# Kernel optimization log

Measured on AMD Instinct MI355X. Metric: run time of the kernel, lower is better.

Reference implementation:

```python
import jax, jax.numpy as jnp
import numpy as np

N = 50000      # nodes
E = 1600000    # edges (before self-loops)
F_IN = 160     # input feature dim
H = 8          # heads
C = 8          # per-head channels
HC = H * C     # 64
G = 64         # graphs in batch
NEG_SLOPE = 0.2


def setup_inputs() -> dict:
    key = jax.random.key(0)
    ks = jax.random.split(key, 20)
    x = jax.random.normal(ks[0], (N, F_IN), jnp.float32)
    edge_index = jax.random.randint(ks[1], (2, E), 0, N, dtype=jnp.int64)
    batch = jnp.sort(jax.random.randint(ks[2], (N,), 0, G, dtype=jnp.int64))

    def w(k, shape):
        fan = shape[0] + shape[-1]
        lim = np.sqrt(6.0 / fan).astype(np.float32)
        return jax.random.uniform(k, shape, jnp.float32, -lim, lim)

    return {
        "x": x, "edge_index": edge_index, "batch": batch,
        "W1": w(ks[3], (F_IN, HC)), "a1s": w(ks[4], (H, C)), "a1d": w(ks[5], (H, C)), "b1": jnp.zeros((HC,), jnp.float32),
        "W2": w(ks[6], (HC, HC)),   "a2s": w(ks[7], (H, C)), "a2d": w(ks[8], (H, C)), "b2": jnp.zeros((HC,), jnp.float32),
        "W3": w(ks[9], (HC, HC)),   "a3s": w(ks[10], (H, C)), "a3d": w(ks[11], (H, C)), "b3": jnp.zeros((HC,), jnp.float32),
        "Wlin": w(ks[12], (HC, 2)), "blin": jnp.zeros((2,), jnp.float32),
    }


def gat_layer(x, src, dst, W, a_src, a_dst, b):
    # h: [N, H, C]
    h = (x @ W).reshape(-1, H, C)
    alpha_src = jnp.einsum('nhc,hc->nh', h, a_src)  # [N, H]
    alpha_dst = jnp.einsum('nhc,hc->nh', h, a_dst)  # [N, H]
    # per-edge scores: message from src j to dst i (PyG convention)
    e = jax.nn.leaky_relu(alpha_src[src] + alpha_dst[dst], NEG_SLOPE)  # [Et, H]
    # softmax over incoming edges of each dst node (numerically stable)
    m = jax.ops.segment_max(e, dst, num_segments=N)
    ex = jnp.exp(e - m[dst])
    s = jax.ops.segment_sum(ex, dst, num_segments=N)
    a = ex / (s[dst] + 1e-16)                                          # [Et, H]
    out = jax.ops.segment_sum(h[src] * a[:, :, None], dst, num_segments=N)
    return out.reshape(-1, HC) + b


def reference(x, edge_index, batch, W1, a1s, a1d, b1, W2, a2s, a2d, b2,
              W3, a3s, a3d, b3, Wlin, blin):
    # add self-loops (PyG GATConv default)
    loop = jnp.arange(N, dtype=edge_index.dtype)
    src = jnp.concatenate([edge_index[0], loop])
    dst = jnp.concatenate([edge_index[1], loop])

    h = jax.nn.elu(gat_layer(x, src, dst, W1, a1s, a1d, b1))
    h = jax.nn.elu(gat_layer(h, src, dst, W2, a2s, a2d, b2))
    h = jax.nn.elu(gat_layer(h, src, dst, W3, a3s, a3d, b3))

    # global mean pool over graphs
    sums = jax.ops.segment_sum(h, batch, num_segments=G)               # [G, HC]
    cnt = jax.ops.segment_sum(jnp.ones((h.shape[0], 1), h.dtype), batch, num_segments=G)
    pooled = sums / jnp.maximum(cnt, 1.0)

    logits = pooled @ Wlin + blin                                      # [G, 2]
    return jax.nn.log_softmax(logits, axis=1)
```

## Files before the change

### kernel.cpp

```cpp
#include <hip/hip_runtime.h>
#include <hip/hip_bf16.h>

#define NNODES 50000
#define NEDGES 1600000
#define F_IN   160
#define NHEAD  8
#define HC     64
#define NGRAPH 64
#define NEG_SLOPE 0.2f

#define BW2   256
#define NB2   ((NNODES + BW2 - 1) / BW2)
#define BCAP  12288
#define EPB   8192
#define PA_BLOCKS ((NEDGES + EPB - 1) / EPB)
#define EPT   (EPB / 256)
#define PCCAP 12288
#define SCAN_BLK 49

__global__ void __launch_bounds__(256) partA_kernel(const int* __restrict__ ei,
                                                    int* __restrict__ bcur,
                                                    unsigned* __restrict__ stage) {
    __shared__ int cnt[NB2];
    __shared__ int rb[NB2];
    __shared__ int gb[NB2];
    __shared__ int sc[256];
    __shared__ unsigned stg[EPB];
    int t = threadIdx.x;
    int e0 = blockIdx.x * EPB;
    for (int i = t; i < NB2; i += 256) cnt[i] = 0;
    __syncthreads();

    unsigned pck[EPT];
#pragma unroll
    for (int i = 0; i < EPT; i++) {
        int e = e0 + i * 256 + t;
        if (e < NEDGES) {
            int s = ei[e];
            int d = ei[NEDGES + e];
            int b = d >> 8;
            pck[i] = (unsigned)s | ((unsigned)(d & 255) << 16) | ((unsigned)b << 24);
            atomicAdd(&cnt[b], 1);
        } else {
            pck[i] = 0xFFFFFFFFu;
        }
    }
    __syncthreads();
    int c = (t < NB2) ? cnt[t] : 0;
    sc[t] = c;
    __syncthreads();
    for (int d = 1; d < 256; d <<= 1) {
        int v = (t >= d) ? sc[t - d] : 0;
        __syncthreads();
        sc[t] += v;
        __syncthreads();
    }
    if (t < NB2) {
        rb[t] = sc[t] - c;
        gb[t] = (c > 0) ? atomicAdd(&bcur[t], c) : 0;
        cnt[t] = 0;
    }
    __syncthreads();
#pragma unroll
    for (int i = 0; i < EPT; i++) {
        int b = pck[i] >> 24;
        if (b < NB2) {
            int p = rb[b] + atomicAdd(&cnt[b], 1);
            stg[p] = pck[i];
        }
    }
    __syncthreads();
    int total = sc[255];
    for (int idx = t; idx < total; idx += 256) {
        unsigned v = stg[idx];
        int b = v >> 24;
        int pos = gb[b] + (idx - rb[b]);
        if (pos < BCAP) stage[(size_t)b * BCAP + pos] = v;
    }
}

__global__ void __launch_bounds__(256) partB_kernel(const unsigned* __restrict__ stage,
                                                    const int* __restrict__ bcur,
                                                    int* __restrict__ deg, int N) {
    __shared__ int cnt[BW2];
    int b = blockIdx.x, t = threadIdx.x;
    cnt[t] = 0;
    __syncthreads();
    int n = bcur[b]; if (n > BCAP) n = BCAP;
    const unsigned* sg = stage + (size_t)b * BCAP;
    for (int i = t; i < n; i += 256) atomicAdd(&cnt[(sg[i] >> 16) & 255], 1);
    __syncthreads();
    int node = b * BW2 + t;
    if (node < N) deg[node] = cnt[t];
}

__global__ void scan_partial_kernel(const int* __restrict__ deg, int* __restrict__ psum, int N) {
    __shared__ int red[256];
    int tid = threadIdx.x;
    int i4 = blockIdx.x * 256 + tid;
    int n4 = N / 4;
    int s = 0;
    if (i4 < n4) {
        int4 v = ((const int4*)deg)[i4];
        s = v.x + v.y + v.z + v.w + 4;
    }
    red[tid] = s;
    __syncthreads();
    for (int d = 128; d > 0; d >>= 1) {
        if (tid < d) red[tid] += red[tid + d];
        __syncthreads();
    }
    if (tid == 0) psum[blockIdx.x] = red[0];
}

__global__ void scan_base_kernel(const int* __restrict__ psum, int* __restrict__ pbase) {
    int lane = threadIdx.x;
    int v = (lane < SCAN_BLK) ? psum[lane] : 0;
    int own = v;
    for (int off = 1; off < 64; off <<= 1) {
        int u = __shfl_up(v, off);
        if (lane >= off) v += u;
    }
    if (lane < SCAN_BLK) pbase[lane] = v - own;
}

__global__ void scan_write_kernel(const int* __restrict__ deg, const int* __restrict__ pbase,
                                  int* __restrict__ row_ptr, int N) {
    __shared__ int red[256];
    int tid = threadIdx.x;
    int b = blockIdx.x;
    int i4 = b * 256 + tid;
    int n4 = N / 4;
    int4 v = make_int4(0, 0, 0, 0);
    int s = 0;
    if (i4 < n4) {
        v = ((const int4*)deg)[i4];
        s = v.x + v.y + v.z + v.w + 4;
    }
    red[tid] = s;
    __syncthreads();
    for (int d = 1; d < 256; d <<= 1) {
        int t2 = (tid >= d) ? red[tid - d] : 0;
        __syncthreads();
        red[tid] += t2;
        __syncthreads();
    }
    if (i4 < n4) {
        int base = pbase[b] + red[tid] - s;
        int gi = i4 * 4;
        int r0 = base + v.x + 1;
        int r1 = r0 + v.y + 1;
        int r2 = r1 + v.z + 1;
        int r3 = r2 + v.w + 1;
        row_ptr[gi + 1] = r0;
        row_ptr[gi + 2] = r1;
        row_ptr[gi + 3] = r2;
        row_ptr[gi + 4] = r3;
        if (gi == 0) row_ptr[0] = 0;
    }
}

__global__ void __launch_bounds__(256) partC_kernel(const unsigned* __restrict__ stage,
                                                    const int* __restrict__ bcur,
                                                    const int* __restrict__ row_ptr,
                                                    int* __restrict__ csr, int N) {
    __shared__ int rstart[BW2 + 1];
    __shared__ int lfill[BW2];
    __shared__ int ord[PCCAP];
    int b = blockIdx.x, t = threadIdx.x;
    int n0 = b * BW2;
    lfill[t] = 0;
    { int n = n0 + t; rstart[t] = row_ptr[n < N ? n : N]; }
    if (t == 0) { int n = n0 + BW2; rstart[BW2] = row_ptr[n < N ? n : N]; }
    __syncthreads();
    int base0 = rstart[0];
    int total = rstart[BW2] - base0;
    int cnt = bcur[b]; if (cnt > BCAP) cnt = BCAP;
    const unsigned* sg = stage + (size_t)b * BCAP;
    if (total <= PCCAP) {
        for (int i = t; i < cnt; i += 256) {
            unsigned v = sg[i];
            int dl = (v >> 16) & 255;
            int p = (rstart[dl] - base0) + atomicAdd(&lfill[dl], 1);
            ord[p] = v & 0xFFFF;
        }
        __syncthreads();
        { int n = n0 + t; if (n < N) ord[rstart[t + 1] - 1 - base0] = n; }
        __syncthreads();
        for (int i = t; i < total; i += 256) csr[base0 + i] = ord[i];
    } else {
        for (int i = t; i < cnt; i += 256) {
            unsigned v = sg[i];
            int dl = (v >> 16) & 255;
            int p = rstart[dl] + atomicAdd(&lfill[dl], 1);
            csr[p] = v & 0xFFFF;
        }
        __syncthreads();
        { int n = n0 + t; if (n < N) csr[rstart[t + 1] - 1] = n; }
    }
}

template <int K, int KC>
__global__ void __launch_bounds__(256) gemm_tile_kernel(const float* __restrict__ in,
                                                        const float* __restrict__ W,
                                                        const float* __restrict__ aS,
                                                        const float* __restrict__ aD,
                                                        __hip_bfloat16* __restrict__ h_out,
                                                        float* __restrict__ alpha_s,
                                                        float* __restrict__ alpha_d,
                                                        int N) {
    __shared__ float xs[64][KC + 1];
    __shared__ float Wl[KC][64];
    int t = threadIdx.x;
    int n0 = blockIdx.x * 64;
    int tn = (t >> 4) << 2;
    int tc = (t & 15) << 2;
    float acc[4][4] = {};

    for (int kc = 0; kc < K; kc += KC) {
        for (int idx = t; idx < 64 * (KC / 4); idx += 256) {
            int n = idx / (KC / 4);
            int k4 = (idx - n * (KC / 4)) * 4;
            int node = n0 + n;
            float4 v = make_float4(0.f, 0.f, 0.f, 0.f);
            if (node < N) v = *reinterpret_cast<const float4*>(&in[(size_t)node * K + kc + k4]);
            xs[n][k4 + 0] = v.x;
            xs[n][k4 + 1] = v.y;
            xs[n][k4 + 2] = v.z;
            xs[n][k4 + 3] = v.w;
        }
        for (int idx = t; idx < KC * 16; idx += 256) {
            int k = idx >> 4;
            int c4 = (idx & 15) << 2;
            *reinterpret_cast<float4*>(&Wl[k][c4]) =
                *reinterpret_cast<const float4*>(&W[(size_t)(kc + k) * HC + c4]);
        }
        __syncthreads();
#pragma unroll 8
        for (int k = 0; k < KC; k++) {
            float x0 = xs[tn + 0][k];
            float x1 = xs[tn + 1][k];
            float x2 = xs[tn + 2][k];
            float x3 = xs[tn + 3][k];
            float4 wv = *reinterpret_cast<const float4*>(&Wl[k][tc]);
            acc[0][0] = fmaf(x0, wv.x, acc[0][0]);
            acc[0][1] = fmaf(x0, wv.y, acc[0][1]);
            acc[0][2] = fmaf(x0, wv.z, acc[0][2]);
            acc[0][3] = fmaf(x0, wv.w, acc[0][3]);
            acc[1][0] = fmaf(x1, wv.x, acc[1][0]);
            acc[1][1] = fmaf(x1, wv.y, acc[1][1]);
            acc[1][2] = fmaf(x1, wv.z, acc[1][2]);
            acc[1][3] = fmaf(x1, wv.w, acc[1][3]);
            acc[2][0] = fmaf(x2, wv.x, acc[2][0]);
            acc[2][1] = fmaf(x2, wv.y, acc[2][1]);
            acc[2][2] = fmaf(x2, wv.z, acc[2][2]);
            acc[2][3] = fmaf(x2, wv.w, acc[2][3]);
            acc[3][0] = fmaf(x3, wv.x, acc[3][0]);
            acc[3][1] = fmaf(x3, wv.y, acc[3][1]);
            acc[3][2] = fmaf(x3, wv.z, acc[3][2]);
            acc[3][3] = fmaf(x3, wv.w, acc[3][3]);
        }
        __syncthreads();
    }

#pragma unroll
    for (int i = 0; i < 4; i++) {
        int node = n0 + tn + i;
        if (node < N) {
            __hip_bfloat16 tmp[4];
            tmp[0] = __float2bfloat16(acc[i][0]);
            tmp[1] = __float2bfloat16(acc[i][1]);
            tmp[2] = __float2bfloat16(acc[i][2]);
            tmp[3] = __float2bfloat16(acc[i][3]);
            *reinterpret_cast<ushort4*>(&h_out[(size_t)node * HC + tc]) =
                *reinterpret_cast<const ushort4*>(tmp);
        }
    }

    float4 aSv = *reinterpret_cast<const float4*>(&aS[tc]);
    float4 aDv = *reinterpret_cast<const float4*>(&aD[tc]);
    float ps[4], pd[4];
#pragma unroll
    for (int i = 0; i < 4; i++) {
        ps[i] = acc[i][0] * aSv.x + acc[i][1] * aSv.y + acc[i][2] * aSv.z + acc[i][3] * aSv.w;
        pd[i] = acc[i][0] * aDv.x + acc[i][1] * aDv.y + acc[i][2] * aDv.z + acc[i][3] * aDv.w;
    }
#pragma unroll
    for (int i = 0; i < 4; i++) {
        ps[i] += __shfl_xor(ps[i], 1);
        pd[i] += __shfl_xor(pd[i], 1);
    }
    if ((t & 1) == 0) {
        int head = (t & 15) >> 1;
#pragma unroll
        for (int i = 0; i < 4; i++) {
            int node = n0 + tn + i;
            if (node < N) {
                alpha_s[node * NHEAD + head] = ps[i];
                alpha_d[node * NHEAD + head] = pd[i];
            }
        }
    }
}

__global__ void __launch_bounds__(256) agg_kernel(const __hip_bfloat16* __restrict__ h,
                           const float* __restrict__ as_, const float* __restrict__ ad_,
                           const int* __restrict__ rowp, const int* __restrict__ csr,
                           const float* __restrict__ bias, float* __restrict__ out, int N) {
    int tid = threadIdx.x;
    int node = blockIdx.x * 4 + (tid >> 6);
    if (node >= N) return;
    int lane = tid & 63;
    int head = lane >> 3;
    int j8 = lane & 7;
    int bl = lane & 56;

    int beg = rowp[node], end = rowp[node + 1];
    int deg = end - beg;
    float adn = ad_[node * NHEAD + head];

    float num0 = 0.f, num1 = 0.f, dent = 0.f;
    int s0safe = csr[beg];
    int ngrp = (deg + 7) >> 3;
    for (int g = 0; g < ngrp; g++) {
        int eidx = g * 8 + j8;
        int sE = s0safe;
        float w_t = 0.f;
        if (eidx < deg) {
            sE = csr[beg + eidx];
            float e = as_[sE * NHEAD + head] + adn;
            e = (e > 0.f) ? e : NEG_SLOPE * e;
            w_t = __expf(e);
        }
        dent += w_t;
#pragma unroll
        for (int j = 0; j < 8; j += 2) {
            int   sa = __shfl(sE, bl + j);
            float wa = __shfl(w_t, bl + j);
            float ha = __bfloat162float(h[(size_t)sa * HC + lane]);
            num0 = fmaf(wa, ha, num0);
            int   sb = __shfl(sE, bl + j + 1);
            float wb = __shfl(w_t, bl + j + 1);
            float hb = __bfloat162float(h[(size_t)sb * HC + lane]);
            num1 = fmaf(wb, hb, num1);
        }
    }
    dent += __shfl_xor(dent, 1);
    dent += __shfl_xor(dent, 2);
    dent += __shfl_xor(dent, 4);
    float o = (num0 + num1) / (dent + 1e-16f) + bias[lane];
    out[node * HC + lane] = (o > 0.f) ? o : (__expf(o) - 1.f);
}

#define PCH 64
__global__ void __launch_bounds__(256) pool_kernel(const float* __restrict__ h,
                                                   const int* __restrict__ batch,
                                                   float* __restrict__ pooled, int N) {
    int tid = threadIdx.x;
    int lane = tid & 63, w = tid >> 6;
    int base = blockIdx.x * PCH + w * (PCH / 4);
    if (base >= N) return;
    int end = base + PCH / 4; if (end > N) end = N;

    int cur = batch[base];
    float acc = 0.f;
    for (int n = base; n < end; n++) {
        int g = batch[n];
        if (g != cur) {
            atomicAdd(&pooled[cur * HC + lane], acc);
            cur = g; acc = 0.f;
        }
        acc += h[(size_t)n * HC + lane];
    }
    atomicAdd(&pooled[cur * HC + lane], acc);
}

__global__ void head_kernel(const float* __restrict__ pooled, const int* __restrict__ batch,
                            const float* __restrict__ Wlin, const float* __restrict__ blin,
                            float* __restrict__ out, int N) {
    int g = threadIdx.x;
    if (g >= NGRAPH) return;
    int lo = 0, hi = N;
    while (lo < hi) { int mid = (lo + hi) >> 1; if (batch[mid] < g) lo = mid + 1; else hi = mid; }
    int start = lo;
    hi = N;
    while (lo < hi) { int mid = (lo + hi) >> 1; if (batch[mid] < g + 1) lo = mid + 1; else hi = mid; }
    float c = fmaxf((float)(lo - start), 1.f);
    float l0 = blin[0], l1 = blin[1];
    for (int k = 0; k < HC; k++) {
        float p = pooled[g * HC + k] / c;
        l0 = fmaf(p, Wlin[k * 2 + 0], l0);
        l1 = fmaf(p, Wlin[k * 2 + 1], l1);
    }
    float mx = fmaxf(l0, l1);
    float lse = mx + logf(expf(l0 - mx) + expf(l1 - mx));
    out[g * 2 + 0] = l0 - lse;
    out[g * 2 + 1] = l1 - lse;
}

extern "C" void kernel_launch(void* const* d_in, const int* in_sizes, int n_in,
                              void* d_out, int out_size, void* d_ws, size_t ws_size,
                              hipStream_t stream) {
    const float* x    = (const float*)d_in[0];
    const int*   ei   = (const int*)d_in[1];
    const int*   batch= (const int*)d_in[2];
    const float* W1   = (const float*)d_in[3];
    const float* a1s  = (const float*)d_in[4];
    const float* a1d  = (const float*)d_in[5];
    const float* b1   = (const float*)d_in[6];
    const float* W2   = (const float*)d_in[7];
    const float* a2s  = (const float*)d_in[8];
    const float* a2d  = (const float*)d_in[9];
    const float* b2   = (const float*)d_in[10];
    const float* W3   = (const float*)d_in[11];
    const float* a3s  = (const float*)d_in[12];
    const float* a3d  = (const float*)d_in[13];
    const float* b3   = (const float*)d_in[14];
    const float* Wlin = (const float*)d_in[15];
    const float* blin = (const float*)d_in[16];
    float* out = (float*)d_out;

    const int N = NNODES, E = NEDGES, Et = E + N;

    char* ws = (char*)d_ws;
    size_t off = 0;
    auto alloc = [&](size_t bytes) { char* p = ws + off; off += (bytes + 255) & ~(size_t)255; return p; };
    int*   row_ptr = (int*)alloc((N + 1) * sizeof(int));
    int*   deg     = (int*)alloc(N * sizeof(int));
    int*   bcur    = (int*)alloc(NB2 * sizeof(int));
    int*   psum    = (int*)alloc(SCAN_BLK * sizeof(int));
    int*   pbase   = (int*)alloc(SCAN_BLK * sizeof(int));
    int*   csr_src = (int*)alloc((size_t)Et * sizeof(int));
    float* as_     = (float*)alloc((size_t)N * NHEAD * sizeof(float));
    float* ad_     = (float*)alloc((size_t)N * NHEAD * sizeof(float));
    __hip_bfloat16* hA = (__hip_bfloat16*)alloc((size_t)N * HC * sizeof(__hip_bfloat16));
    float* hB      = (float*)alloc((size_t)N * HC * sizeof(float));
    float* pooled  = (float*)alloc(NGRAPH * HC * sizeof(float));
    unsigned int* stage = (unsigned int*)hB;

    hipMemsetAsync(bcur, 0, NB2 * sizeof(int), stream);
    partA_kernel<<<PA_BLOCKS, 256, 0, stream>>>(ei, bcur, stage);
    partB_kernel<<<NB2, 256, 0, stream>>>(stage, bcur, deg, N);
    scan_partial_kernel<<<SCAN_BLK, 256, 0, stream>>>(deg, psum, N);
    scan_base_kernel<<<1, 64, 0, stream>>>(psum, pbase);
    scan_write_kernel<<<SCAN_BLK, 256, 0, stream>>>(deg, pbase, row_ptr, N);
    partC_kernel<<<NB2, 256, 0, stream>>>(stage, bcur, row_ptr, csr_src, N);

    int nodeBlocks = (N + 3) / 4;
    int tileBlocks = (N + 63) / 64;

    gemm_tile_kernel<F_IN, 80><<<tileBlocks, 256, 0, stream>>>(x, W1, a1s, a1d, hA, as_, ad_, N);
    agg_kernel<<<nodeBlocks, 256, 0, stream>>>(hA, as_, ad_, row_ptr, csr_src, b1, hB, N);

    gemm_tile_kernel<HC, 64><<<tileBlocks, 256, 0, stream>>>(hB, W2, a2s, a2d, hA, as_, ad_, N);
    agg_kernel<<<nodeBlocks, 256, 0, stream>>>(hA, as_, ad_, row_ptr, csr_src, b2, hB, N);

    gemm_tile_kernel<HC, 64><<<tileBlocks, 256, 0, stream>>>(hB, W3, a3s, a3d, hA, as_, ad_, N);
    agg_kernel<<<nodeBlocks, 256, 0, stream>>>(hA, as_, ad_, row_ptr, csr_src, b3, hB, N);

    hipMemsetAsync(pooled, 0, NGRAPH * HC * sizeof(float), stream);
    pool_kernel<<<(N + PCH - 1) / PCH, 256, 0, stream>>>(hB, batch, pooled, N);
    head_kernel<<<1, 64, 0, stream>>>(pooled, batch, Wlin, blin, out, N);
}
```

Measured before the change: 386.2 us.

## Pack source index and bf16 weight into one shuffle; scan bucket counts directly

The aggregation kernel now packs each edge's 16-bit source id and bf16-rounded softmax weight into one 32-bit word. This halves the cross-lane shuffles, and the loop processes two 8-edge groups per iteration to put more gathers in flight. The prefix-sum stage drops the partial-reduction kernel and instead scans per-bucket edge counts from bcur, removing one launch. The risks are that source ids only fit in 16 bits while N=50000 stays under 65536, and that weights are rounded to bf16 precision.

```diff
diff --git a/kernel.cpp b/kernel.cpp
--- a/kernel.cpp
+++ b/kernel.cpp
@@ -16,7 +16,6 @@
 #define PA_BLOCKS ((NEDGES + EPB - 1) / EPB)
 #define EPT   (EPB / 256)
 #define PCCAP 12288
-#define SCAN_BLK 49
 
 __global__ void __launch_bounds__(256) partA_kernel(const int* __restrict__ ei,
                                                     int* __restrict__ bcur,
@@ -94,70 +93,44 @@
     if (node < N) deg[node] = cnt[t];
 }
 
-__global__ void scan_partial_kernel(const int* __restrict__ deg, int* __restrict__ psum, int N) {
-    __shared__ int red[256];
-    int tid = threadIdx.x;
-    int i4 = blockIdx.x * 256 + tid;
-    int n4 = N / 4;
-    int s = 0;
-    if (i4 < n4) {
-        int4 v = ((const int4*)deg)[i4];
-        s = v.x + v.y + v.z + v.w + 4;
-    }
-    red[tid] = s;
-    __syncthreads();
-    for (int d = 128; d > 0; d >>= 1) {
-        if (tid < d) red[tid] += red[tid + d];
-        __syncthreads();
-    }
-    if (tid == 0) psum[blockIdx.x] = red[0];
-}
-
-__global__ void scan_base_kernel(const int* __restrict__ psum, int* __restrict__ pbase) {
-    int lane = threadIdx.x;
-    int v = (lane < SCAN_BLK) ? psum[lane] : 0;
-    int own = v;
-    for (int off = 1; off < 64; off <<= 1) {
-        int u = __shfl_up(v, off);
-        if (lane >= off) v += u;
-    }
-    if (lane < SCAN_BLK) pbase[lane] = v - own;
-}
-
-__global__ void scan_write_kernel(const int* __restrict__ deg, const int* __restrict__ pbase,
-                                  int* __restrict__ row_ptr, int N) {
-    __shared__ int red[256];
-    int tid = threadIdx.x;
-    int b = blockIdx.x;
-    int i4 = b * 256 + tid;
-    int n4 = N / 4;
-    int4 v = make_int4(0, 0, 0, 0);
-    int s = 0;
-    if (i4 < n4) {
-        v = ((const int4*)deg)[i4];
-        s = v.x + v.y + v.z + v.w + 4;
-    }
-    red[tid] = s;
+__global__ void __launch_bounds__(256) scan_base_kernel(const int* __restrict__ bcur,
+                                                        int* __restrict__ pbase, int N) {
+    __shared__ int sc[256];
+    int t = threadIdx.x;
+    int tot = 0;
+    if (t < NB2) {
+        int c = bcur[t]; if (c > BCAP) c = BCAP;
+        int nodes = N - t * BW2; if (nodes > BW2) nodes = BW2; if (nodes < 0) nodes = 0;
+        tot = c + nodes;
+    }
+    sc[t] = tot;
     __syncthreads();
     for (int d = 1; d < 256; d <<= 1) {
-        int t2 = (tid >= d) ? red[tid - d] : 0;
-        __syncthreads();
-        red[tid] += t2;
-        __syncthreads();
-    }
-    if (i4 < n4) {
-        int base = pbase[b] + red[tid] - s;
-        int gi = i4 * 4;
-        int r0 = base + v.x + 1;
-        int r1 = r0 + v.y + 1;
-        int r2 = r1 + v.z + 1;
-        int r3 = r2 + v.w + 1;
-        row_ptr[gi + 1] = r0;
-        row_ptr[gi + 2] = r1;
-        row_ptr[gi + 3] = r2;
-        row_ptr[gi + 4] = r3;
-        if (gi == 0) row_ptr[0] = 0;
-    }
+        int v = (t >= d) ? sc[t - d] : 0;
+        __syncthreads();
+        sc[t] += v;
+        __syncthreads();
+    }
+    if (t < NB2) pbase[t] = sc[t] - tot;
+}
+
+__global__ void __launch_bounds__(256) scan_write_kernel(const int* __restrict__ deg,
+                                                         const int* __restrict__ pbase,
+                                                         int* __restrict__ row_ptr, int N) {
+    __shared__ int sc[256];
+    int b = blockIdx.x, t = threadIdx.x;
+    int n = b * BW2 + t;
+    int d = (n < N) ? deg[n] + 1 : 0;
+    sc[t] = d;
+    __syncthreads();
+    for (int s = 1; s < 256; s <<= 1) {
+        int v = (t >= s) ? sc[t - s] : 0;
+        __syncthreads();
+        sc[t] += v;
+        __syncthreads();
+    }
+    if (n < N) row_ptr[n + 1] = pbase[b] + sc[t];
+    if (b == 0 && t == 0) row_ptr[0] = 0;
 }
 
 __global__ void __launch_bounds__(256) partC_kernel(const unsigned* __restrict__ stage,
@@ -303,6 +276,12 @@
     }
 }
 
+__device__ __forceinline__ unsigned packsw(int s, float w) {
+    unsigned u = __float_as_uint(w);
+    u = (u + 0x7FFFu + ((u >> 16) & 1u)) & 0xFFFF0000u;
+    return u | (unsigned)s;
+}
+
 __global__ void __launch_bounds__(256) agg_kernel(const __hip_bfloat16* __restrict__ h,
                            const float* __restrict__ as_, const float* __restrict__ ad_,
                            const int* __restrict__ rowp, const int* __restrict__ csr,
@@ -318,31 +297,60 @@
     int beg = rowp[node], end = rowp[node + 1];
     int deg = end - beg;
     float adn = ad_[node * NHEAD + head];
+    unsigned uSafe = (unsigned)csr[beg];
 
     float num0 = 0.f, num1 = 0.f, dent = 0.f;
-    int s0safe = csr[beg];
     int ngrp = (deg + 7) >> 3;
-    for (int g = 0; g < ngrp; g++) {
-        int eidx = g * 8 + j8;
-        int sE = s0safe;
-        float w_t = 0.f;
-        if (eidx < deg) {
-            sE = csr[beg + eidx];
-            float e = as_[sE * NHEAD + head] + adn;
+    int g = 0;
+    for (; g + 1 < ngrp; g += 2) {
+        int e1 = g * 8 + j8;
+        int e2 = e1 + 8;
+        unsigned uA = uSafe, uB = uSafe;
+        if (e1 < deg) {
+            int s = csr[beg + e1];
+            float e = as_[s * NHEAD + head] + adn;
             e = (e > 0.f) ? e : NEG_SLOPE * e;
-            w_t = __expf(e);
-        }
-        dent += w_t;
-#pragma unroll
-        for (int j = 0; j < 8; j += 2) {
-            int   sa = __shfl(sE, bl + j);
-            float wa = __shfl(w_t, bl + j);
-            float ha = __bfloat162float(h[(size_t)sa * HC + lane]);
-            num0 = fmaf(wa, ha, num0);
-            int   sb = __shfl(sE, bl + j + 1);
-            float wb = __shfl(w_t, bl + j + 1);
-            float hb = __bfloat162float(h[(size_t)sb * HC + lane]);
-            num1 = fmaf(wb, hb, num1);
+            float w = __expf(e);
+            dent += w;
+            uA = packsw(s, w);
+        }
+        if (e2 < deg) {
+            int s = csr[beg + e2];
+            float e = as_[s * NHEAD + head] + adn;
+            e = (e > 0.f) ? e : NEG_SLOPE * e;
+            float w = __expf(e);
+            dent += w;
+            uB = packsw(s, w);
+        }
+#pragma unroll
+        for (int j = 0; j < 8; j++) {
+            unsigned va = __shfl(uA, bl + j);
+            unsigned vb = __shfl(uB, bl + j);
+            float wa = __uint_as_float(va & 0xFFFF0000u);
+            float wb = __uint_as_float(vb & 0xFFFF0000u);
+            int   sa = va & 0xFFFF;
+            int   sb = vb & 0xFFFF;
+            num0 = fmaf(wa, __bfloat162float(h[(size_t)sa * HC + lane]), num0);
+            num1 = fmaf(wb, __bfloat162float(h[(size_t)sb * HC + lane]), num1);
+        }
+    }
+    for (; g < ngrp; g++) {
+        int e1 = g * 8 + j8;
+        unsigned uA = uSafe;
+        if (e1 < deg) {
+            int s = csr[beg + e1];
+            float e = as_[s * NHEAD + head] + adn;
+            e = (e > 0.f) ? e : NEG_SLOPE * e;
+            float w = __expf(e);
+            dent += w;
+            uA = packsw(s, w);
+        }
+#pragma unroll
+        for (int j = 0; j < 8; j++) {
+            unsigned va = __shfl(uA, bl + j);
+            float wa = __uint_as_float(va & 0xFFFF0000u);
+            int   sa = va & 0xFFFF;
+            num0 = fmaf(wa, __bfloat162float(h[(size_t)sa * HC + lane]), num0);
         }
     }
     dent += __shfl_xor(dent, 1);
@@ -428,8 +436,7 @@
     int*   row_ptr = (int*)alloc((N + 1) * sizeof(int));
     int*   deg     = (int*)alloc(N * sizeof(int));
     int*   bcur    = (int*)alloc(NB2 * sizeof(int));
-    int*   psum    = (int*)alloc(SCAN_BLK * sizeof(int));
-    int*   pbase   = (int*)alloc(SCAN_BLK * sizeof(int));
+    int*   pbase   = (int*)alloc(NB2 * sizeof(int));
     int*   csr_src = (int*)alloc((size_t)Et * sizeof(int));
     float* as_     = (float*)alloc((size_t)N * NHEAD * sizeof(float));
     float* ad_     = (float*)alloc((size_t)N * NHEAD * sizeof(float));
@@ -441,9 +448,8 @@
     hipMemsetAsync(bcur, 0, NB2 * sizeof(int), stream);
     partA_kernel<<<PA_BLOCKS, 256, 0, stream>>>(ei, bcur, stage);
     partB_kernel<<<NB2, 256, 0, stream>>>(stage, bcur, deg, N);
-    scan_partial_kernel<<<SCAN_BLK, 256, 0, stream>>>(deg, psum, N);
-    scan_base_kernel<<<1, 64, 0, stream>>>(psum, pbase);
-    scan_write_kernel<<<SCAN_BLK, 256, 0, stream>>>(deg, pbase, row_ptr, N);
+    scan_base_kernel<<<1, 256, 0, stream>>>(bcur, pbase, N);
+    scan_write_kernel<<<NB2, 256, 0, stream>>>(deg, pbase, row_ptr, N);
     partC_kernel<<<NB2, 256, 0, stream>>>(stage, bcur, row_ptr, csr_src, N);
 
     int nodeBlocks = (N + 3) / 4;
```

Result: faster. 374.5 us (-3.0%).
